# Optimization experiments

Hardware: AMD Instinct MI355X
Metric: run time of the kernel (lower is better)

## Reference

```python
import jax, jax.numpy as jnp
import numpy as np
import math

NUM_HEADS = 16
HEAD_DIM = 64
ROPE_BASE = 10000.0

def _rope_tables(T, dtype):
    # inv_freq: (D/2,), emb = cat([freqs, freqs]) -> (T, D)
    inv_freq = 1.0 / (ROPE_BASE ** (jnp.arange(0, HEAD_DIM, 2, dtype=jnp.float32) / HEAD_DIM))
    t = jnp.arange(T, dtype=jnp.float32)
    freqs = jnp.einsum('i,j->ij', t, inv_freq)          # (T, D/2)
    emb = jnp.concatenate([freqs, freqs], axis=-1)      # (T, D)
    return jnp.cos(emb).astype(dtype), jnp.sin(emb).astype(dtype)

def _rotate_half(x):
    # interleaved pair rotation: (x0,x1,x2,x3,...) -> (-x1,x0,-x3,x2,...)
    x1 = x[..., ::2]
    x2 = x[..., 1::2]
    return jnp.stack((-x2, x1), axis=-1).reshape(x.shape)

def setup_inputs() -> dict:
    key = jax.random.key(0)
    ks = jax.random.split(key, 9)
    B, T, C = 2, 2048, 1024
    s = 1.0 / math.sqrt(C)
    return {
        'x':  jax.random.normal(ks[0], (B, T, C), dtype=jnp.float32),
        'wq': jax.random.normal(ks[1], (C, C), dtype=jnp.float32) * s,
        'bq': jax.random.normal(ks[2], (C,), dtype=jnp.float32) * s,
        'wk': jax.random.normal(ks[3], (C, C), dtype=jnp.float32) * s,
        'bk': jax.random.normal(ks[4], (C,), dtype=jnp.float32) * s,
        'wv': jax.random.normal(ks[5], (C, C), dtype=jnp.float32) * s,
        'bv': jax.random.normal(ks[6], (C,), dtype=jnp.float32) * s,
        'wo': jax.random.normal(ks[7], (C, C), dtype=jnp.float32) * s,
        'bo': jax.random.normal(ks[8], (C,), dtype=jnp.float32) * s,
    }

def reference(x, wq, bq, wk, bk, wv, bv, wo, bo):
    B, T, C = x.shape
    H, D = NUM_HEADS, HEAD_DIM

    def heads(t):  # (B,T,C) -> (B,H,T,D)
        return t.reshape(B, T, H, D).transpose(0, 2, 1, 3)

    q = heads(x @ wq.T + bq)
    k = heads(x @ wk.T + bk)
    v = heads(x @ wv.T + bv)

    cos, sin = _rope_tables(T, x.dtype)                 # (T, D)
    cos = cos[None, None]                               # (1,1,T,D)
    sin = sin[None, None]
    q = q * cos + _rotate_half(q) * sin
    k = k * cos + _rotate_half(k) * sin

    scores = jnp.einsum('bhqd,bhkd->bhqk', q, k) / math.sqrt(D)
    attn = jax.nn.softmax(scores, axis=-1)
    out = jnp.einsum('bhqk,bhkd->bhqd', attn, v)        # (B,H,T,D)
    out = out.transpose(0, 2, 1, 3).reshape(B, T, C)
    return out @ wo.T + bo
```

## Files before the change

### kernel.cpp

```cpp
#include <hip/hip_runtime.h>
#include <cmath>

#define TSEQ 2048
#define CDIM 1024
#define NHEAD 16
#define HDIM 64

typedef _Float16 half8 __attribute__((ext_vector_type(8)));
typedef _Float16 half4 __attribute__((ext_vector_type(4)));
typedef __fp16 fp16x2 __attribute__((ext_vector_type(2)));
typedef float f32x4 __attribute__((ext_vector_type(4)));
typedef float f32x16 __attribute__((ext_vector_type(16)));
typedef unsigned int u32x4 __attribute__((ext_vector_type(4)));

#define QSCALE   0.18033688011112042f
#define SHIFT_L2 12.984255368000671f

__device__ __forceinline__ void gload16(const void* g, void* l) {
    __builtin_amdgcn_global_load_lds((const __attribute__((address_space(1))) void*)g,
                                     (__attribute__((address_space(3))) void*)l, 16, 0, 0);
}

__device__ __forceinline__ unsigned int cvtpk_u32(float a, float b) {
    fp16x2 r = __builtin_amdgcn_cvt_pkrtz(a, b);
    return __builtin_bit_cast(unsigned int, r);
}

__device__ __forceinline__ void plane_swap(unsigned int& a, unsigned int& b) {
    asm("v_permlane32_swap_b32 %0, %1" : "+v"(a), "+v"(b));
}

__global__ __launch_bounds__(256) void cvt_kernel(
    const float* __restrict__ x, const float* __restrict__ wq, const float* __restrict__ wk,
    const float* __restrict__ wv, const float* __restrict__ wo, _Float16* __restrict__ dst)
{
    const int y = blockIdx.y;
    const float* src;
    size_t cnt, doff;
    if (y == 0) { src = x; cnt = 4194304; doff = 0; }
    else {
        cnt = 1048576; doff = 4194304 + (size_t)(y - 1) * 1048576;
        src = (y == 1) ? wq : (y == 2) ? wk : (y == 3) ? wv : wo;
    }
    size_t i = ((size_t)blockIdx.x * 256 + threadIdx.x) * 4;
    if (i >= cnt) return;
    const float4 v = *(const float4*)(src + i);
    half4 h;
    h[0] = (_Float16)v.x; h[1] = (_Float16)v.y; h[2] = (_Float16)v.z; h[3] = (_Float16)v.w;
    *(half4*)(dst + doff + i) = h;
}

__global__ __launch_bounds__(256) void qkv_mfma_kernel(
    const _Float16* __restrict__ xh,
    const _Float16* __restrict__ wqh, const _Float16* __restrict__ wkh, const _Float16* __restrict__ wvh,
    const float* __restrict__ bq, const float* __restrict__ bk, const float* __restrict__ bv,
    _Float16* __restrict__ Qh, _Float16* __restrict__ Kh, _Float16* __restrict__ Vth)
{
    __shared__ __align__(16) _Float16 As[2 * 64 * 64];
    __shared__ __align__(16) _Float16 Bs[2 * 128 * 64];
    const int tid = threadIdx.x;
    const int lane = tid & 63, wid = tid >> 6;
    const int z = blockIdx.z;
    const _Float16* wh = (z == 0) ? wqh : (z == 1) ? wkh : wvh;
    const int m0 = blockIdx.y << 6, n0 = blockIdx.x << 7;

    const int srow = tid >> 3;
    const int sch = ((tid & 7) ^ (srow & 7)) * 8;
    const _Float16* gA = xh + (size_t)(m0 + srow) * CDIM + sch;
    const _Float16* gB = wh + (size_t)(n0 + srow) * CDIM + sch;
    _Float16* lA = As + tid * 8;
    _Float16* lB = Bs + tid * 8;

    const int cq = lane & 15, kg = lane >> 4;
    const int cx = cq & 7;

    f32x4 acc[4][2] = {};

    gload16(gA, lA);                 gload16(gA + (size_t)32 * CDIM, lA + 2048);
    gload16(gB, lB);                 gload16(gB + (size_t)32 * CDIM, lB + 2048);
    gload16(gB + (size_t)64 * CDIM, lB + 4096);
    gload16(gB + (size_t)96 * CDIM, lB + 6144);
    __syncthreads();

    for (int k0 = 0; k0 < CDIM; k0 += 64) {
        const int buf = (k0 >> 6) & 1;
        if (k0 + 64 < CDIM) {
            const int na = (buf ^ 1) * 4096, nb = (buf ^ 1) * 8192;
            gload16(gA + k0 + 64, lA + na);
            gload16(gA + (size_t)32 * CDIM + k0 + 64, lA + na + 2048);
            gload16(gB + k0 + 64, lB + nb);
            gload16(gB + (size_t)32 * CDIM + k0 + 64, lB + nb + 2048);
            gload16(gB + (size_t)64 * CDIM + k0 + 64, lB + nb + 4096);
            gload16(gB + (size_t)96 * CDIM + k0 + 64, lB + nb + 6144);
        }
        const _Float16* Ab = As + buf * 4096;
        const _Float16* Bb = Bs + buf * 8192;

        half8 af[4][2], bf[2][2];
#pragma unroll
        for (int i = 0; i < 4; ++i)
#pragma unroll
            for (int ks = 0; ks < 2; ++ks)
                af[i][ks] = *(const half8*)(Ab + (i * 16 + cq) * 64 + (((4 * ks + kg)) ^ cx) * 8);
#pragma unroll
        for (int j = 0; j < 2; ++j)
#pragma unroll
            for (int ks = 0; ks < 2; ++ks)
                bf[j][ks] = *(const half8*)(Bb + (wid * 32 + j * 16 + cq) * 64 + (((4 * ks + kg)) ^ cx) * 8);

        __builtin_amdgcn_s_setprio(1);
#pragma unroll
        for (int ks = 0; ks < 2; ++ks)
#pragma unroll
            for (int i = 0; i < 4; ++i)
#pragma unroll
                for (int j = 0; j < 2; ++j)
                    acc[i][j] = __builtin_amdgcn_mfma_f32_16x16x32_f16(af[i][ks], bf[j][ks], acc[i][j], 0, 0, 0);
        __builtin_amdgcn_s_setprio(0);
        __syncthreads();
    }

    if (z < 2) {
        const float* bias = z ? bk : bq;
        _Float16* dst = z ? Kh : Qh;
        const float qs = z ? 1.f : QSCALE;
#pragma unroll
        for (int fn = 0; fn < 2; ++fn) {
            int n = n0 + wid * 32 + fn * 16 + cq;
            int d = n & 63, h = n >> 6;
            float bs = bias[n];
            float fr = exp2f((float)(d & 31) * -0.41524101186092029f);
            float sgn = (d & 1) ? 1.f : -1.f;
#pragma unroll
            for (int fm = 0; fm < 4; ++fm) {
#pragma unroll
                for (int r = 0; r < 4; ++r) {
                    int m = m0 + fm * 16 + (kg << 2) + r;
                    int t = m & (TSEQ - 1), b = m >> 11;
                    float v = acc[fm][fn][r] + bs;
                    float prt = __shfl_xor(v, 1);
                    float sn, cs;
                    __sincosf((float)t * fr, &sn, &cs);
                    dst[(((size_t)(b * NHEAD + h)) * TSEQ + t) * HDIM + d] =
                        (_Float16)((v * cs + sgn * prt * sn) * qs);
                }
            }
        }
    } else {
#pragma unroll
        for (int fn = 0; fn < 2; ++fn) {
            int n = n0 + wid * 32 + fn * 16 + cq;
            int d = n & 63, h = n >> 6;
            float bs = bv[n];
#pragma unroll
            for (int fm = 0; fm < 4; ++fm) {
                int m = m0 + fm * 16 + (kg << 2);
                int t = m & (TSEQ - 1), b = m >> 11;
                half4 ov;
#pragma unroll
                for (int r = 0; r < 4; ++r) ov[r] = (_Float16)(acc[fm][fn][r] + bs);
                *(half4*)&Vth[(((size_t)(b * NHEAD + h)) * HDIM + d) * TSEQ + t] = ov;
            }
        }
    }
}

__global__ __launch_bounds__(512, 4) void attn_mfma_kernel(
    const _Float16* __restrict__ Qh, const _Float16* __restrict__ Kh,
    const _Float16* __restrict__ Vth, _Float16* __restrict__ Ah)
{
    __shared__ __align__(16) _Float16 Ks[2 * 2 * 64 * 64];
    __shared__ __align__(16) _Float16 Vts[2 * 2 * 64 * 64];

    const int tid = threadIdx.x, lane = tid & 63, wid = tid >> 6;
    const int lin = blockIdx.x + 16 * blockIdx.y;
    const int idx = lin >> 3;
    const int bh = (lin & 7) * 4 + (idx & 3);
    const int q0 = (idx >> 2) << 7;
    const size_t hb = (size_t)bh * TSEQ * HDIM;

    const int ql = lane & 31;
    const int hi = lane >> 5;
    const int lx = lane & 7;
    const int qt = wid & 3;
    const int kh = wid >> 2;
    const int koff = kh << 10;

    const int qrow = q0 + qt * 32 + ql;
    const _Float16* gq = Qh + hb + (size_t)qrow * HDIM + hi * 8;
    half8 bQ[4];
#pragma unroll
    for (int ks = 0; ks < 4; ++ks) bQ[ks] = *(const half8*)(gq + ks * 16);

    const int srow = qt * 8 + (lane >> 3);
    const int sch = ((lane & 7) ^ (srow & 7)) * 8;
    const _Float16* gKs = Kh + hb + (size_t)(koff + srow) * HDIM + sch;
    const _Float16* gVs = Vth + hb + (size_t)srow * TSEQ + koff + sch;
    _Float16* lKs = Ks + kh * 8192 + qt * 512 + lane * 8;
    _Float16* lVs = Vts + kh * 8192 + qt * 512 + lane * 8;

    f32x16 o0 = {}, o1 = {};
    float l_run = 0.f;
    f32x16 sinit;
#pragma unroll
    for (int i = 0; i < 16; ++i) sinit[i] = -SHIFT_L2;

    gload16(gKs, lKs);                  gload16(gKs + 32 * HDIM, lKs + 2048);
    gload16(gVs, lVs);                  gload16(gVs + 32 * TSEQ, lVs + 2048);
    __syncthreads();

    for (int kt = 0; kt < 16; ++kt) {
        const int buf = kt & 1;
        if (kt + 1 < 16) {
            const int nb = (buf ^ 1) * 4096;
            gload16(gKs + (size_t)(kt + 1) * 4096, lKs + nb);
            gload16(gKs + (size_t)(kt + 1) * 4096 + 32 * HDIM, lKs + nb + 2048);
            gload16(gVs + (kt + 1) * 64, lVs + nb);
            gload16(gVs + (kt + 1) * 64 + 32 * TSEQ, lVs + nb + 2048);
        }
        const _Float16* Kb = Ks + kh * 8192 + buf * 4096;
        const _Float16* Vb = Vts + kh * 8192 + buf * 4096;

        f32x16 s0 = sinit, s1 = sinit;
        __builtin_amdgcn_s_setprio(1);
#pragma unroll
        for (int ks = 0; ks < 4; ++ks) {
            half8 k0 = *(const half8*)(Kb + ql * 64 + ((2 * ks + hi) ^ lx) * 8);
            half8 k1 = *(const half8*)(Kb + (32 + ql) * 64 + ((2 * ks + hi) ^ lx) * 8);
            s0 = __builtin_amdgcn_mfma_f32_32x32x16_f16(k0, bQ[ks], s0, 0, 0, 0);
            s1 = __builtin_amdgcn_mfma_f32_32x32x16_f16(k1, bQ[ks], s1, 0, 0, 0);
        }
        __builtin_amdgcn_s_setprio(0);

        f32x16 p0, p1;
#pragma unroll
        for (int i = 0; i < 16; ++i) p0[i] = __builtin_amdgcn_exp2f(s0[i]);
#pragma unroll
        for (int i = 0; i < 16; ++i) p1[i] = __builtin_amdgcn_exp2f(s1[i]);
        float ls = 0.f;
#pragma unroll
        for (int i = 0; i < 16; ++i) ls += p0[i] + p1[i];
        l_run += ls;

        half8 bP[4];
#pragma unroll
        for (int g = 0; g < 2; ++g) {
            const f32x16& p = g ? p1 : p0;
            unsigned int a0 = cvtpk_u32(p[0], p[1]),   a1 = cvtpk_u32(p[2], p[3]);
            unsigned int b0 = cvtpk_u32(p[4], p[5]),   b1 = cvtpk_u32(p[6], p[7]);
            unsigned int c0 = cvtpk_u32(p[8], p[9]),   c1 = cvtpk_u32(p[10], p[11]);
            unsigned int d0 = cvtpk_u32(p[12], p[13]), d1 = cvtpk_u32(p[14], p[15]);
            plane_swap(a0, b0);
            plane_swap(a1, b1);
            plane_swap(c0, d0);
            plane_swap(c1, d1);
            u32x4 w0 = { a0, a1, b0, b1 };
            u32x4 w1 = { c0, c1, d0, d1 };
            bP[2 * g]     = __builtin_bit_cast(half8, w0);
            bP[2 * g + 1] = __builtin_bit_cast(half8, w1);
        }

        __builtin_amdgcn_s_setprio(1);
#pragma unroll
        for (int ks = 0; ks < 4; ++ks) {
            half8 v0 = *(const half8*)(Vb + ql * 64 + ((2 * ks + hi) ^ lx) * 8);
            half8 v1 = *(const half8*)(Vb + (32 + ql) * 64 + ((2 * ks + hi) ^ lx) * 8);
            o0 = __builtin_amdgcn_mfma_f32_32x32x16_f16(v0, bP[ks], o0, 0, 0, 0);
            o1 = __builtin_amdgcn_mfma_f32_32x32x16_f16(v1, bP[ks], o1, 0, 0, 0);
        }
        __builtin_amdgcn_s_setprio(0);
        __syncthreads();
    }

    const float l_half = l_run + __shfl_xor(l_run, 32);
    float* Ored = (float*)Ks;
    float* Lsum = (float*)Vts;

    if (kh == 1) {
#pragma unroll
        for (int dg = 0; dg < 2; ++dg) {
            const f32x16& o = dg ? o1 : o0;
#pragma unroll
            for (int r = 0; r < 16; ++r) {
                int d = dg * 32 + (r & 3) + 8 * (r >> 2) + 4 * hi;
                Ored[qt * 2048 + d * 32 + ql] = o[r];
            }
        }
        if (!hi) Lsum[qt * 32 + ql] = l_half;
    }
    __syncthreads();
    if (kh == 0) {
        const int b = bh >> 4, hh = bh & 15;
        const float inv = 1.f / (l_half + Lsum[qt * 32 + ql]);
        const size_t rowoff = ((size_t)b * TSEQ + qrow) * CDIM + hh * 64;
#pragma unroll
        for (int dg = 0; dg < 2; ++dg) {
            const f32x16& o = dg ? o1 : o0;
#pragma unroll
            for (int j = 0; j < 4; ++j) {
                half4 ov;
#pragma unroll
                for (int c = 0; c < 4; ++c) {
                    int d = dg * 32 + 8 * j + 4 * hi + c;
                    ov[c] = (_Float16)((o[4 * j + c] + Ored[qt * 2048 + d * 32 + ql]) * inv);
                }
                *(half4*)&Ah[rowoff + dg * 32 + j * 8 + hi * 4] = ov;
            }
        }
    }
}

__global__ __launch_bounds__(256) void oproj_mfma_kernel(
    const _Float16* __restrict__ Ahh, const _Float16* __restrict__ woh,
    const float* __restrict__ bo, float* __restrict__ out)
{
    __shared__ __align__(16) _Float16 As[2 * 64 * 64];
    __shared__ __align__(16) _Float16 Bs[2 * 128 * 64];
    const int tid = threadIdx.x;
    const int lane = tid & 63, wid = tid >> 6;
    const int m0 = blockIdx.y << 6, n0 = blockIdx.x << 7;

    const int srow = tid >> 3;
    const int sch = ((tid & 7) ^ (srow & 7)) * 8;
    const _Float16* gA = Ahh + (size_t)(m0 + srow) * CDIM + sch;
    const _Float16* gB = woh + (size_t)(n0 + srow) * CDIM + sch;
    _Float16* lA = As + tid * 8;
    _Float16* lB = Bs + tid * 8;

    const int cq = lane & 15, kg = lane >> 4;
    const int cx = cq & 7;

    f32x4 acc[4][2] = {};

    gload16(gA, lA);                 gload16(gA + (size_t)32 * CDIM, lA + 2048);
    gload16(gB, lB);                 gload16(gB + (size_t)32 * CDIM, lB + 2048);
    gload16(gB + (size_t)64 * CDIM, lB + 4096);
    gload16(gB + (size_t)96 * CDIM, lB + 6144);
    __syncthreads();

    for (int k0 = 0; k0 < CDIM; k0 += 64) {
        const int buf = (k0 >> 6) & 1;
        if (k0 + 64 < CDIM) {
            const int na = (buf ^ 1) * 4096, nb = (buf ^ 1) * 8192;
            gload16(gA + k0 + 64, lA + na);
            gload16(gA + (size_t)32 * CDIM + k0 + 64, lA + na + 2048);
            gload16(gB + k0 + 64, lB + nb);
            gload16(gB + (size_t)32 * CDIM + k0 + 64, lB + nb + 2048);
            gload16(gB + (size_t)64 * CDIM + k0 + 64, lB + nb + 4096);
            gload16(gB + (size_t)96 * CDIM + k0 + 64, lB + nb + 6144);
        }
        const _Float16* Ab = As + buf * 4096;
        const _Float16* Bb = Bs + buf * 8192;

        half8 af[4][2], bf[2][2];
#pragma unroll
        for (int i = 0; i < 4; ++i)
#pragma unroll
            for (int ks = 0; ks < 2; ++ks)
                af[i][ks] = *(const half8*)(Ab + (i * 16 + cq) * 64 + (((4 * ks + kg)) ^ cx) * 8);
#pragma unroll
        for (int j = 0; j < 2; ++j)
#pragma unroll
            for (int ks = 0; ks < 2; ++ks)
                bf[j][ks] = *(const half8*)(Bb + (wid * 32 + j * 16 + cq) * 64 + (((4 * ks + kg)) ^ cx) * 8);

        __builtin_amdgcn_s_setprio(1);
#pragma unroll
        for (int ks = 0; ks < 2; ++ks)
#pragma unroll
            for (int i = 0; i < 4; ++i)
#pragma unroll
                for (int j = 0; j < 2; ++j)
                    acc[i][j] = __builtin_amdgcn_mfma_f32_16x16x32_f16(af[i][ks], bf[j][ks], acc[i][j], 0, 0, 0);
        __builtin_amdgcn_s_setprio(0);
        __syncthreads();
    }

#pragma unroll
    for (int fn = 0; fn < 2; ++fn) {
        int n = n0 + wid * 32 + fn * 16 + cq;
        float bs = bo[n];
#pragma unroll
        for (int fm = 0; fm < 4; ++fm) {
#pragma unroll
            for (int r = 0; r < 4; ++r) {
                int m = m0 + fm * 16 + (kg << 2) + r;
                out[(size_t)m * CDIM + n] = acc[fm][fn][r] + bs;
            }
        }
    }
}

extern "C" void kernel_launch(void* const* d_in, const int* in_sizes, int n_in,
                              void* d_out, int out_size, void* d_ws, size_t ws_size,
                              hipStream_t stream) {
    (void)in_sizes; (void)n_in; (void)out_size; (void)ws_size;
    const float* x  = (const float*)d_in[0];
    const float* wq = (const float*)d_in[1];
    const float* bq = (const float*)d_in[2];
    const float* wk = (const float*)d_in[3];
    const float* bk = (const float*)d_in[4];
    const float* wv = (const float*)d_in[5];
    const float* bv = (const float*)d_in[6];
    const float* wo = (const float*)d_in[7];
    const float* bo = (const float*)d_in[8];
    float* out = (float*)d_out;

    _Float16* xh  = (_Float16*)d_ws;
    _Float16* wqh = xh + 4194304;
    _Float16* wkh = wqh + 1048576;
    _Float16* wvh = wkh + 1048576;
    _Float16* woh = wvh + 1048576;
    _Float16* Qh  = woh + 1048576;
    _Float16* Kh  = Qh + 4194304;
    _Float16* Vth = Kh + 4194304;
    _Float16* Ah  = Vth + 4194304;

    cvt_kernel<<<dim3(4096, 5), 256, 0, stream>>>(x, wq, wk, wv, wo, xh);
    qkv_mfma_kernel<<<dim3(8, 64, 3), 256, 0, stream>>>(xh, wqh, wkh, wvh, bq, bk, bv, Qh, Kh, Vth);
    attn_mfma_kernel<<<dim3(16, 32), 512, 0, stream>>>(Qh, Kh, Vth, Ah);
    oproj_mfma_kernel<<<dim3(8, 64), 256, 0, stream>>>(Ah, woh, bo, out);
}
```

Baseline: 117.6 us.

## Retile QKV GEMM to 128x128 block tiles with 2x2 warp grid and K=32

The QKV projection kernel moves from 64x128 block tiles with K-step 64 to 128x128 tiles with K-step 32. Each of the four waves now computes a 64x64 sub-tile (4x4 MFMA accumulators) in a 2x2 wave grid, and the LDS swizzle is changed to match the 32-wide rows. The grid is halved in M, and launch bounds request 3 blocks per CU. The goal is more arithmetic per LDS/global load and fewer blocks, at the cost of more accumulator registers and twice as many K-loop iterations and barriers.

```diff
diff --git a/kernel.cpp b/kernel.cpp
--- a/kernel.cpp
+++ b/kernel.cpp
@@ -50,72 +50,63 @@
     *(half4*)(dst + doff + i) = h;
 }
 
-__global__ __launch_bounds__(256) void qkv_mfma_kernel(
+__global__ __launch_bounds__(256, 3) void qkv_mfma_kernel(
     const _Float16* __restrict__ xh,
     const _Float16* __restrict__ wqh, const _Float16* __restrict__ wkh, const _Float16* __restrict__ wvh,
     const float* __restrict__ bq, const float* __restrict__ bk, const float* __restrict__ bv,
     _Float16* __restrict__ Qh, _Float16* __restrict__ Kh, _Float16* __restrict__ Vth)
 {
-    __shared__ __align__(16) _Float16 As[2 * 64 * 64];
-    __shared__ __align__(16) _Float16 Bs[2 * 128 * 64];
+    __shared__ __align__(16) _Float16 As[2 * 128 * 32];
+    __shared__ __align__(16) _Float16 Bs[2 * 128 * 32];
     const int tid = threadIdx.x;
     const int lane = tid & 63, wid = tid >> 6;
+    const int wr = wid >> 1, wc = wid & 1;
     const int z = blockIdx.z;
     const _Float16* wh = (z == 0) ? wqh : (z == 1) ? wkh : wvh;
-    const int m0 = blockIdx.y << 6, n0 = blockIdx.x << 7;
-
-    const int srow = tid >> 3;
-    const int sch = ((tid & 7) ^ (srow & 7)) * 8;
+    const int m0 = blockIdx.y << 7, n0 = blockIdx.x << 7;
+
+    const int srow = tid >> 2;
+    const int sch = ((tid & 3) ^ ((srow >> 1) & 3)) * 8;
     const _Float16* gA = xh + (size_t)(m0 + srow) * CDIM + sch;
     const _Float16* gB = wh + (size_t)(n0 + srow) * CDIM + sch;
-    _Float16* lA = As + tid * 8;
-    _Float16* lB = Bs + tid * 8;
 
     const int cq = lane & 15, kg = lane >> 4;
-    const int cx = cq & 7;
-
-    f32x4 acc[4][2] = {};
-
-    gload16(gA, lA);                 gload16(gA + (size_t)32 * CDIM, lA + 2048);
-    gload16(gB, lB);                 gload16(gB + (size_t)32 * CDIM, lB + 2048);
-    gload16(gB + (size_t)64 * CDIM, lB + 4096);
-    gload16(gB + (size_t)96 * CDIM, lB + 6144);
+    const int rchunk = (kg ^ ((lane >> 1) & 3)) * 8;
+    const _Float16* pA0 = As + (wr * 64 + cq) * 32 + rchunk;
+    const _Float16* pB0 = Bs + (wc * 64 + cq) * 32 + rchunk;
+
+    f32x4 acc[4][4] = {};
+
+    gload16(gA, As + tid * 8);
+    gload16(gA + (size_t)64 * CDIM, As + 2048 + tid * 8);
+    gload16(gB, Bs + tid * 8);
+    gload16(gB + (size_t)64 * CDIM, Bs + 2048 + tid * 8);
     __syncthreads();
 
-    for (int k0 = 0; k0 < CDIM; k0 += 64) {
-        const int buf = (k0 >> 6) & 1;
-        if (k0 + 64 < CDIM) {
-            const int na = (buf ^ 1) * 4096, nb = (buf ^ 1) * 8192;
-            gload16(gA + k0 + 64, lA + na);
-            gload16(gA + (size_t)32 * CDIM + k0 + 64, lA + na + 2048);
-            gload16(gB + k0 + 64, lB + nb);
-            gload16(gB + (size_t)32 * CDIM + k0 + 64, lB + nb + 2048);
-            gload16(gB + (size_t)64 * CDIM + k0 + 64, lB + nb + 4096);
-            gload16(gB + (size_t)96 * CDIM + k0 + 64, lB + nb + 6144);
-        }
-        const _Float16* Ab = As + buf * 4096;
-        const _Float16* Bb = Bs + buf * 8192;
-
-        half8 af[4][2], bf[2][2];
+    for (int k0 = 0; k0 < CDIM; k0 += 32) {
+        const int buf = (k0 >> 5) & 1;
+        if (k0 + 32 < CDIM) {
+            const int nb = (buf ^ 1) * 4096;
+            gload16(gA + k0 + 32, As + nb + tid * 8);
+            gload16(gA + (size_t)64 * CDIM + k0 + 32, As + nb + 2048 + tid * 8);
+            gload16(gB + k0 + 32, Bs + nb + tid * 8);
+            gload16(gB + (size_t)64 * CDIM + k0 + 32, Bs + nb + 2048 + tid * 8);
+        }
+        const _Float16* pA = pA0 + buf * 4096;
+        const _Float16* pB = pB0 + buf * 4096;
+
+        half8 af[4], bf[4];
+#pragma unroll
+        for (int f = 0; f < 4; ++f) {
+            af[f] = *(const half8*)(pA + f * 512);
+            bf[f] = *(const half8*)(pB + f * 512);
+        }
+        __builtin_amdgcn_s_setprio(1);
 #pragma unroll
         for (int i = 0; i < 4; ++i)
 #pragma unroll
-            for (int ks = 0; ks < 2; ++ks)
-                af[i][ks] = *(const half8*)(Ab + (i * 16 + cq) * 64 + (((4 * ks + kg)) ^ cx) * 8);
-#pragma unroll
-        for (int j = 0; j < 2; ++j)
-#pragma unroll
-            for (int ks = 0; ks < 2; ++ks)
-                bf[j][ks] = *(const half8*)(Bb + (wid * 32 + j * 16 + cq) * 64 + (((4 * ks + kg)) ^ cx) * 8);
-
-        __builtin_amdgcn_s_setprio(1);
-#pragma unroll
-        for (int ks = 0; ks < 2; ++ks)
-#pragma unroll
-            for (int i = 0; i < 4; ++i)
-#pragma unroll
-                for (int j = 0; j < 2; ++j)
-                    acc[i][j] = __builtin_amdgcn_mfma_f32_16x16x32_f16(af[i][ks], bf[j][ks], acc[i][j], 0, 0, 0);
+            for (int j = 0; j < 4; ++j)
+                acc[i][j] = __builtin_amdgcn_mfma_f32_16x16x32_f16(af[i], bf[j], acc[i][j], 0, 0, 0);
         __builtin_amdgcn_s_setprio(0);
         __syncthreads();
     }
@@ -125,8 +116,8 @@
         _Float16* dst = z ? Kh : Qh;
         const float qs = z ? 1.f : QSCALE;
 #pragma unroll
-        for (int fn = 0; fn < 2; ++fn) {
-            int n = n0 + wid * 32 + fn * 16 + cq;
+        for (int fn = 0; fn < 4; ++fn) {
+            int n = n0 + wc * 64 + fn * 16 + cq;
             int d = n & 63, h = n >> 6;
             float bs = bias[n];
             float fr = exp2f((float)(d & 31) * -0.41524101186092029f);
@@ -135,7 +126,7 @@
             for (int fm = 0; fm < 4; ++fm) {
 #pragma unroll
                 for (int r = 0; r < 4; ++r) {
-                    int m = m0 + fm * 16 + (kg << 2) + r;
+                    int m = m0 + wr * 64 + fm * 16 + (kg << 2) + r;
                     int t = m & (TSEQ - 1), b = m >> 11;
                     float v = acc[fm][fn][r] + bs;
                     float prt = __shfl_xor(v, 1);
@@ -148,13 +139,13 @@
         }
     } else {
 #pragma unroll
-        for (int fn = 0; fn < 2; ++fn) {
-            int n = n0 + wid * 32 + fn * 16 + cq;
+        for (int fn = 0; fn < 4; ++fn) {
+            int n = n0 + wc * 64 + fn * 16 + cq;
             int d = n & 63, h = n >> 6;
             float bs = bv[n];
 #pragma unroll
             for (int fm = 0; fm < 4; ++fm) {
-                int m = m0 + fm * 16 + (kg << 2);
+                int m = m0 + wr * 64 + fm * 16 + (kg << 2);
                 int t = m & (TSEQ - 1), b = m >> 11;
                 half4 ov;
 #pragma unroll
@@ -417,7 +408,7 @@
     _Float16* Ah  = Vth + 4194304;
 
     cvt_kernel<<<dim3(4096, 5), 256, 0, stream>>>(x, wq, wk, wv, wo, xh);
-    qkv_mfma_kernel<<<dim3(8, 64, 3), 256, 0, stream>>>(xh, wqh, wkh, wvh, bq, bk, bv, Qh, Kh, Vth);
+    qkv_mfma_kernel<<<dim3(8, 32, 3), 256, 0, stream>>>(xh, wqh, wkh, wvh, bq, bk, bv, Qh, Kh, Vth);
     attn_mfma_kernel<<<dim3(16, 32), 512, 0, stream>>>(Qh, Kh, Vth, Ah);
     oproj_mfma_kernel<<<dim3(8, 64), 256, 0, stream>>>(Ah, woh, bo, out);
 }
```

Measured after the change: 113.2 us. 3.8% less time.
